# Performance work log

Measured on AMD Instinct MI355X. Metric: run time of the kernel, lower is better.

Reference implementation:

```python
import jax, jax.numpy as jnp
import numpy as np

TEMPERATURE = 0.5
EPS = 1e-12  # matches torch F.normalize clamp_min


def setup_inputs() -> dict:
    key = jax.random.key(0)
    k1, k2 = jax.random.split(key)
    N, D, C = 8192, 128, 64
    out_1 = jax.random.normal(k1, (N, D), dtype=jnp.float32)
    label = jax.random.randint(k2, (N,), 0, C, dtype=jnp.int64)
    return {"out_1": out_1, "label": label}


def reference(out_1, label):
    N = out_1.shape[0]
    # L2 normalize rows (F.normalize with eps clamp)
    norm = jnp.maximum(jnp.linalg.norm(out_1, axis=-1, keepdims=True), EPS)
    x = out_1 / norm
    # exp-scaled cosine similarity matrix [N, N]
    sim = jnp.exp(jnp.matmul(x, x.T) / TEMPERATURE)
    not_diag = 1.0 - jnp.eye(N, dtype=sim.dtype)
    # negatives: all off-diagonal entries per row
    negative_sim = jnp.sum(sim * not_diag, axis=-1)
    # positives: same label, excluding self; mean per row
    pos_mask = (label[:, None] == label[None, :]).astype(sim.dtype) * not_diag
    pos_count = jnp.sum(pos_mask, axis=-1)
    pos_sim = jnp.sum(sim * pos_mask, axis=-1) / pos_count
    return jnp.mean(-jnp.log(pos_sim / negative_sim))
```

## Files before the change

### kernel.cpp

```cpp
#include <hip/hip_runtime.h>
#include <hip/hip_bf16.h>
#include <stdint.h>

typedef __attribute__((ext_vector_type(8))) __bf16 bf16x8;
typedef __attribute__((ext_vector_type(16))) float floatx16;

#if __has_builtin(__builtin_amdgcn_exp2f)
#define EXP2F(x) __builtin_amdgcn_exp2f(x)
#else
#define EXP2F(x) exp2f(x)
#endif

#define GAS __attribute__((address_space(1)))
#define LAS __attribute__((address_space(3)))

#define SCALE_SQRT 1.69864359f
#define JCH 8

__global__ __launch_bounds__(256) void k_prep(const float* __restrict__ x,
                                              const int* __restrict__ raw,
                                              ushort* __restrict__ xb,
                                              int* __restrict__ lab, int N) {
  const int row = (blockIdx.x * 256 + threadIdx.x) >> 6;
  const int lane = threadIdx.x & 63;
  if (row >= N) return;
  const int probe = raw[2 * lane + 1];
  const bool is64 = (__ballot(probe != 0) == 0ull);
  const float2 v = ((const float2*)(x + (size_t)row * 128))[lane];
  float ss = v.x * v.x + v.y * v.y;
#pragma unroll
  for (int m = 1; m < 64; m <<= 1) ss += __shfl_xor(ss, m, 64);
  const float rn = SCALE_SQRT / fmaxf(sqrtf(ss), 1e-12f);
  __hip_bfloat162 o;
  o.x = __float2bfloat16(v.x * rn);
  o.y = __float2bfloat16(v.y * rn);
  ((__hip_bfloat162*)xb)[row * 64 + lane] = o;
  if (lane == 0) lab[row] = is64 ? raw[2 * row] : raw[row];
}

__global__ __launch_bounds__(256, 2) void k_sim(const ushort* __restrict__ xb,
                                                const int* __restrict__ lab,
                                                float* __restrict__ pneg,
                                                float* __restrict__ ppos,
                                                int N, int jpb) {
  __shared__ ushort ldsB[2][64 * 128];
  const int tid = threadIdx.x;
  const int lane = tid & 63;
  const int wv = tid >> 6;
  const int l31 = lane & 31, g2 = lane >> 5;
  const int l15 = lane & 15, g4 = lane >> 4;
  const int i0 = blockIdx.y * 128;
  const int c = blockIdx.x;
  const int jt0 = c * jpb;

  {
    const int j0 = jt0 * 64;
#pragma unroll
    for (int it = 0; it < 4; ++it) {
      const int r0 = it * 16 + wv * 4;
      const int lr = r0 + g4;
      const int kb = l15 ^ (lr & 15);
      const ushort* gp = xb + (size_t)(j0 + lr) * 128 + kb * 8;
      __builtin_amdgcn_global_load_lds((GAS void*)gp, (LAS void*)&ldsB[0][r0 * 128], 16, 0, 0);
    }
  }

  const int arow = i0 + wv * 32 + l31;
  bf16x8 af[8];
#pragma unroll
  for (int kt = 0; kt < 8; ++kt)
    af[kt] = *(const bf16x8*)(xb + (size_t)arow * 128 + (kt * 2 + g2) * 8);

  int li[16];
  float neg[16], pos[16];
#pragma unroll
  for (int r = 0; r < 16; ++r) {
    li[r] = lab[i0 + wv * 32 + (r & 3) + 8 * (r >> 2) + 4 * g2];
    neg[r] = 0.0f;
    pos[r] = 0.0f;
  }
  __syncthreads();

  for (int t = 0; t < jpb; ++t) {
    const int j0 = (jt0 + t) * 64;
    const int buf = t & 1;
    if (t + 1 < jpb) {
      const int jn = j0 + 64;
#pragma unroll
      for (int it = 0; it < 4; ++it) {
        const int r0 = it * 16 + wv * 4;
        const int lr = r0 + g4;
        const int kb = l15 ^ (lr & 15);
        const ushort* gp = xb + (size_t)(jn + lr) * 128 + kb * 8;
        __builtin_amdgcn_global_load_lds((GAS void*)gp, (LAS void*)&ldsB[buf ^ 1][r0 * 128], 16, 0, 0);
      }
    }
    const int lj0 = lab[j0 + l31];
    const int lj1 = lab[j0 + 32 + l31];

    floatx16 acc[2];
    acc[0] = (floatx16)(0.0f);
    acc[1] = (floatx16)(0.0f);
    __builtin_amdgcn_s_setprio(1);
#pragma unroll
    for (int kt = 0; kt < 8; ++kt) {
#pragma unroll
      for (int h = 0; h < 2; ++h) {
        const int brow = h * 32 + l31;
        const int bkb = (kt * 2 + g2) ^ (brow & 15);
        const bf16x8 bfr = *(const bf16x8*)&ldsB[buf][brow * 128 + bkb * 8];
        acc[h] = __builtin_amdgcn_mfma_f32_32x32x16_bf16(af[kt], bfr, acc[h], 0, 0, 0);
      }
    }
    __builtin_amdgcn_s_setprio(0);

    const int dlt = j0 - i0;
    const bool diag = ((unsigned)dlt < 128u);
    auto epi = [&](bool DG) {
#pragma unroll
      for (int h = 0; h < 2; ++h) {
        const int lj = h ? lj1 : lj0;
        const int jc = h * 32 + l31 + dlt;
#pragma unroll
        for (int r = 0; r < 16; ++r) {
          float e = EXP2F(acc[h][r]);
          if (DG) {
            const int ir = wv * 32 + (r & 3) + 8 * (r >> 2) + 4 * g2;
            if (ir == jc) e = 0.0f;
          }
          neg[r] += e;
          pos[r] += (li[r] == lj) ? e : 0.0f;
        }
      }
    };
    if (diag) epi(true); else epi(false);
    __syncthreads();
  }

#pragma unroll
  for (int r = 0; r < 16; ++r) {
    float n = neg[r], p = pos[r];
#pragma unroll
    for (int m = 1; m < 32; m <<= 1) {
      n += __shfl_xor(n, m, 64);
      p += __shfl_xor(p, m, 64);
    }
    if (l31 == 0) {
      const int row = i0 + wv * 32 + (r & 3) + 8 * (r >> 2) + 4 * g2;
      pneg[(size_t)c * N + row] = n;
      ppos[(size_t)c * N + row] = p;
    }
  }
}

__global__ __launch_bounds__(256) void k_final(const float* __restrict__ pneg,
                                               const float* __restrict__ ppos,
                                               const int* __restrict__ lab,
                                               double* __restrict__ partial, int N) {
  __shared__ int h[64];
  __shared__ double wsum[4];
  const int tid = threadIdx.x;
  if (tid < 64) h[tid] = 0;
  __syncthreads();
  for (int i = tid; i < N; i += 256) atomicAdd(&h[lab[i] & 63], 1);
  __syncthreads();
  const int r = blockIdx.x * 256 + tid;
  double v = 0.0;
  if (r < N) {
    float n = 0.0f, p = 0.0f;
#pragma unroll
    for (int cc = 0; cc < JCH; ++cc) {
      n += pneg[(size_t)cc * N + r];
      p += ppos[(size_t)cc * N + r];
    }
    const float cnt = (float)(h[lab[r] & 63] - 1);
    v = (double)logf(n * cnt / p);
  }
#pragma unroll
  for (int m = 1; m < 64; m <<= 1) v += __shfl_xor(v, m, 64);
  if ((tid & 63) == 0) wsum[tid >> 6] = v;
  __syncthreads();
  if (tid == 0) partial[blockIdx.x] = wsum[0] + wsum[1] + wsum[2] + wsum[3];
}

__global__ __launch_bounds__(64) void k_write(const double* __restrict__ partial,
                                              float* __restrict__ out, int nfb, int N) {
  const int l = threadIdx.x;
  double v = 0.0;
  for (int i = l; i < nfb; i += 64) v += partial[i];
#pragma unroll
  for (int m = 1; m < 64; m <<= 1) v += __shfl_xor(v, m, 64);
  if (l == 0) out[0] = (float)(v / (double)N);
}

extern "C" void kernel_launch(void* const* d_in, const int* in_sizes, int n_in,
                              void* d_out, int out_size, void* d_ws, size_t ws_size,
                              hipStream_t stream) {
  const float* x = (const float*)d_in[0];
  const int* raw_label = (const int*)d_in[1];
  const int N = in_sizes[1];
  char* ws = (char*)d_ws;
  ushort* xb = (ushort*)ws;
  float* pneg = (float*)(ws + (size_t)N * 128 * 2);
  float* ppos = pneg + (size_t)JCH * N;
  int* lab = (int*)(ppos + (size_t)JCH * N);
  double* partial = (double*)(lab + N);
  float* out = (float*)d_out;

  const int jpb = (N / 64) / JCH;
  const int nfb = (N + 255) / 256;

  k_prep<<<dim3(N / 4), dim3(256), 0, stream>>>(x, raw_label, xb, lab, N);
  k_sim<<<dim3(JCH, N / 128), dim3(256), 0, stream>>>(xb, lab, pneg, ppos, N, jpb);
  k_final<<<dim3(nfb), dim3(256), 0, stream>>>(pneg, ppos, lab, partial, N);
  k_write<<<dim3(1), dim3(64), 0, stream>>>(partial, out, nfb, N);
}
```

Before: 98.06 us.

## Exploit symmetry of similarity matrix by computing only upper-triangular tile pairs

```diff
diff --git a/kernel.cpp b/kernel.cpp
--- a/kernel.cpp
+++ b/kernel.cpp
@@ -15,7 +15,6 @@
 #define LAS __attribute__((address_space(3)))
 
 #define SCALE_SQRT 1.69864359f
-#define JCH 8
 
 __global__ __launch_bounds__(256) void k_prep(const float* __restrict__ x,
                                               const int* __restrict__ raw,
@@ -42,27 +41,29 @@
                                                 const int* __restrict__ lab,
                                                 float* __restrict__ pneg,
                                                 float* __restrict__ ppos,
-                                                int N, int jpb) {
-  __shared__ ushort ldsB[2][64 * 128];
+                                                int N) {
+  __shared__ ushort ldsB[128 * 128];
   const int tid = threadIdx.x;
   const int lane = tid & 63;
   const int wv = tid >> 6;
   const int l31 = lane & 31, g2 = lane >> 5;
   const int l15 = lane & 15, g4 = lane >> 4;
-  const int i0 = blockIdx.y * 128;
-  const int c = blockIdx.x;
-  const int jt0 = c * jpb;
-
-  {
-    const int j0 = jt0 * 64;
-#pragma unroll
-    for (int it = 0; it < 4; ++it) {
-      const int r0 = it * 16 + wv * 4;
-      const int lr = r0 + g4;
-      const int kb = l15 ^ (lr & 15);
-      const ushort* gp = xb + (size_t)(j0 + lr) * 128 + kb * 8;
-      __builtin_amdgcn_global_load_lds((GAS void*)gp, (LAS void*)&ldsB[0][r0 * 128], 16, 0, 0);
-    }
+
+  const int bid = blockIdx.x;
+  int u = (int)((sqrtf(8.0f * (float)bid + 1.0f) - 1.0f) * 0.5f);
+  while ((u + 1) * (u + 2) / 2 <= bid) ++u;
+  while (u * (u + 1) / 2 > bid) --u;
+  const int s = bid - u * (u + 1) / 2;
+  const int i0 = s * 128;
+  const int jb0 = u * 128;
+
+#pragma unroll
+  for (int it = 0; it < 8; ++it) {
+    const int r0 = it * 16 + wv * 4;
+    const int lr = r0 + g4;
+    const int kb = l15 ^ (lr & 15);
+    const ushort* gp = xb + (size_t)(jb0 + lr) * 128 + kb * 8;
+    __builtin_amdgcn_global_load_lds((GAS void*)gp, (LAS void*)&ldsB[r0 * 128], 16, 0, 0);
   }
 
   const int arow = i0 + wv * 32 + l31;
@@ -79,22 +80,13 @@
     neg[r] = 0.0f;
     pos[r] = 0.0f;
   }
-  __syncthreads();
-
-  for (int t = 0; t < jpb; ++t) {
-    const int j0 = (jt0 + t) * 64;
-    const int buf = t & 1;
-    if (t + 1 < jpb) {
-      const int jn = j0 + 64;
-#pragma unroll
-      for (int it = 0; it < 4; ++it) {
-        const int r0 = it * 16 + wv * 4;
-        const int lr = r0 + g4;
-        const int kb = l15 ^ (lr & 15);
-        const ushort* gp = xb + (size_t)(jn + lr) * 128 + kb * 8;
-        __builtin_amdgcn_global_load_lds((GAS void*)gp, (LAS void*)&ldsB[buf ^ 1][r0 * 128], 16, 0, 0);
-      }
-    }
+  const bool offd = (u != s);
+  __syncthreads();
+
+  float cnT[2][2], cpT[2][2];
+#pragma unroll
+  for (int tile = 0; tile < 2; ++tile) {
+    const int j0 = jb0 + tile * 64;
     const int lj0 = lab[j0 + l31];
     const int lj1 = lab[j0 + 32 + l31];
 
@@ -106,17 +98,31 @@
     for (int kt = 0; kt < 8; ++kt) {
 #pragma unroll
       for (int h = 0; h < 2; ++h) {
-        const int brow = h * 32 + l31;
+        const int brow = tile * 64 + h * 32 + l31;
         const int bkb = (kt * 2 + g2) ^ (brow & 15);
-        const bf16x8 bfr = *(const bf16x8*)&ldsB[buf][brow * 128 + bkb * 8];
+        const bf16x8 bfr = *(const bf16x8*)&ldsB[brow * 128 + bkb * 8];
         acc[h] = __builtin_amdgcn_mfma_f32_32x32x16_bf16(af[kt], bfr, acc[h], 0, 0, 0);
       }
     }
     __builtin_amdgcn_s_setprio(0);
 
-    const int dlt = j0 - i0;
-    const bool diag = ((unsigned)dlt < 128u);
-    auto epi = [&](bool DG) {
+    float cn0 = 0.0f, cn1 = 0.0f, cp0 = 0.0f, cp1 = 0.0f;
+    if (offd) {
+#pragma unroll
+      for (int h = 0; h < 2; ++h) {
+        const int lj = h ? lj1 : lj0;
+#pragma unroll
+        for (int r = 0; r < 16; ++r) {
+          const float e = EXP2F(acc[h][r]);
+          const bool mt = (li[r] == lj);
+          neg[r] += e;
+          pos[r] += mt ? e : 0.0f;
+          if (h) { cn1 += e; cp1 += mt ? e : 0.0f; }
+          else   { cn0 += e; cp0 += mt ? e : 0.0f; }
+        }
+      }
+    } else {
+      const int dlt = tile * 64;
 #pragma unroll
       for (int h = 0; h < 2; ++h) {
         const int lj = h ? lj1 : lj0;
@@ -124,17 +130,15 @@
 #pragma unroll
         for (int r = 0; r < 16; ++r) {
           float e = EXP2F(acc[h][r]);
-          if (DG) {
-            const int ir = wv * 32 + (r & 3) + 8 * (r >> 2) + 4 * g2;
-            if (ir == jc) e = 0.0f;
-          }
+          const int ir = wv * 32 + (r & 3) + 8 * (r >> 2) + 4 * g2;
+          if (ir == jc) e = 0.0f;
           neg[r] += e;
           pos[r] += (li[r] == lj) ? e : 0.0f;
         }
       }
-    };
-    if (diag) epi(true); else epi(false);
-    __syncthreads();
+    }
+    cnT[tile][0] = cn0; cnT[tile][1] = cn1;
+    cpT[tile][0] = cp0; cpT[tile][1] = cp1;
   }
 
 #pragma unroll
@@ -147,16 +151,46 @@
     }
     if (l31 == 0) {
       const int row = i0 + wv * 32 + (r & 3) + 8 * (r >> 2) + 4 * g2;
-      pneg[(size_t)c * N + row] = n;
-      ppos[(size_t)c * N + row] = p;
-    }
+      pneg[(size_t)u * N + row] = n;
+      ppos[(size_t)u * N + row] = p;
+    }
+  }
+
+  if (offd) {
+    __syncthreads();
+    float* cb = (float*)ldsB;
+#pragma unroll
+    for (int tile = 0; tile < 2; ++tile) {
+#pragma unroll
+      for (int h = 0; h < 2; ++h) {
+        float a = cnT[tile][h] + __shfl_xor(cnT[tile][h], 32, 64);
+        float b = cpT[tile][h] + __shfl_xor(cpT[tile][h], 32, 64);
+        if (lane < 32) {
+          cb[(((wv * 2 + tile) * 2 + h) * 2 + 0) * 32 + l31] = a;
+          cb[(((wv * 2 + tile) * 2 + h) * 2 + 1) * 32 + l31] = b;
+        }
+      }
+    }
+    __syncthreads();
+    const int c5 = tid & 31;
+    const int np = (tid >> 5) & 1;
+    const int h = (tid >> 6) & 1;
+    const int t = (tid >> 7) & 1;
+    float v = 0.0f;
+#pragma unroll
+    for (int w = 0; w < 4; ++w)
+      v += cb[(((w * 2 + t) * 2 + h) * 2 + np) * 32 + c5];
+    const int jrow = jb0 + t * 64 + h * 32 + c5;
+    if (np == 0) pneg[(size_t)s * N + jrow] = v;
+    else         ppos[(size_t)s * N + jrow] = v;
   }
 }
 
 __global__ __launch_bounds__(256) void k_final(const float* __restrict__ pneg,
                                                const float* __restrict__ ppos,
                                                const int* __restrict__ lab,
-                                               double* __restrict__ partial, int N) {
+                                               double* __restrict__ partial,
+                                               int N, int nstrip) {
   __shared__ int h[64];
   __shared__ double wsum[4];
   const int tid = threadIdx.x;
@@ -168,8 +202,8 @@
   double v = 0.0;
   if (r < N) {
     float n = 0.0f, p = 0.0f;
-#pragma unroll
-    for (int cc = 0; cc < JCH; ++cc) {
+#pragma unroll 8
+    for (int cc = 0; cc < nstrip; ++cc) {
       n += pneg[(size_t)cc * N + r];
       p += ppos[(size_t)cc * N + r];
     }
@@ -199,19 +233,20 @@
   const float* x = (const float*)d_in[0];
   const int* raw_label = (const int*)d_in[1];
   const int N = in_sizes[1];
+  const int nstrip = N / 128;
   char* ws = (char*)d_ws;
   ushort* xb = (ushort*)ws;
   float* pneg = (float*)(ws + (size_t)N * 128 * 2);
-  float* ppos = pneg + (size_t)JCH * N;
-  int* lab = (int*)(ppos + (size_t)JCH * N);
+  float* ppos = pneg + (size_t)nstrip * N;
+  int* lab = (int*)(ppos + (size_t)nstrip * N);
   double* partial = (double*)(lab + N);
   float* out = (float*)d_out;
 
-  const int jpb = (N / 64) / JCH;
+  const int pairs = nstrip * (nstrip + 1) / 2;
   const int nfb = (N + 255) / 256;
 
   k_prep<<<dim3(N / 4), dim3(256), 0, stream>>>(x, raw_label, xb, lab, N);
-  k_sim<<<dim3(JCH, N / 128), dim3(256), 0, stream>>>(xb, lab, pneg, ppos, N, jpb);
-  k_final<<<dim3(nfb), dim3(256), 0, stream>>>(pneg, ppos, lab, partial, N);
+  k_sim<<<dim3(pairs), dim3(256), 0, stream>>>(xb, lab, pneg, ppos, N);
+  k_final<<<dim3(nfb), dim3(256), 0, stream>>>(pneg, ppos, lab, partial, N, nstrip);
   k_write<<<dim3(1), dim3(64), 0, stream>>>(partial, out, nfb, N);
 }
```

Measured after the change: 101.5 us. +3.5%, slower.

## Pack labels to bytes, vectorize accumulators, raise occupancy and j-split count

Applied to the files above, without the earlier changes.

```diff
diff --git a/kernel.cpp b/kernel.cpp
--- a/kernel.cpp
+++ b/kernel.cpp
@@ -15,12 +15,13 @@
 #define LAS __attribute__((address_space(3)))
 
 #define SCALE_SQRT 1.69864359f
-#define JCH 8
+#define JCH 32
 
 __global__ __launch_bounds__(256) void k_prep(const float* __restrict__ x,
                                               const int* __restrict__ raw,
                                               ushort* __restrict__ xb,
-                                              int* __restrict__ lab, int N) {
+                                              unsigned char* __restrict__ lab8,
+                                              int N) {
   const int row = (blockIdx.x * 256 + threadIdx.x) >> 6;
   const int lane = threadIdx.x & 63;
   if (row >= N) return;
@@ -35,13 +36,12 @@
   o.x = __float2bfloat16(v.x * rn);
   o.y = __float2bfloat16(v.y * rn);
   ((__hip_bfloat162*)xb)[row * 64 + lane] = o;
-  if (lane == 0) lab[row] = is64 ? raw[2 * row] : raw[row];
-}
-
-__global__ __launch_bounds__(256, 2) void k_sim(const ushort* __restrict__ xb,
-                                                const int* __restrict__ lab,
-                                                float* __restrict__ pneg,
-                                                float* __restrict__ ppos,
+  if (lane == 0) lab8[row] = (unsigned char)(is64 ? raw[2 * row] : raw[row]);
+}
+
+__global__ __launch_bounds__(256, 4) void k_sim(const ushort* __restrict__ xb,
+                                                const unsigned char* __restrict__ lab8,
+                                                float2* __restrict__ ppart,
                                                 int N, int jpb) {
   __shared__ ushort ldsB[2][64 * 128];
   const int tid = threadIdx.x;
@@ -71,14 +71,13 @@
   for (int kt = 0; kt < 8; ++kt)
     af[kt] = *(const bf16x8*)(xb + (size_t)arow * 128 + (kt * 2 + g2) * 8);
 
-  int li[16];
-  float neg[16], pos[16];
-#pragma unroll
-  for (int r = 0; r < 16; ++r) {
-    li[r] = lab[i0 + wv * 32 + (r & 3) + 8 * (r >> 2) + 4 * g2];
-    neg[r] = 0.0f;
-    pos[r] = 0.0f;
-  }
+  const uint* lab32 = (const uint*)lab8;
+  uint liw[4];
+#pragma unroll
+  for (int q = 0; q < 4; ++q)
+    liw[q] = lab32[(i0 + wv * 32 + 8 * q + 4 * g2) >> 2];
+
+  floatx16 vneg = (floatx16)(0.0f), vpos = (floatx16)(0.0f);
   __syncthreads();
 
   for (int t = 0; t < jpb; ++t) {
@@ -95,42 +94,39 @@
         __builtin_amdgcn_global_load_lds((GAS void*)gp, (LAS void*)&ldsB[buf ^ 1][r0 * 128], 16, 0, 0);
       }
     }
-    const int lj0 = lab[j0 + l31];
-    const int lj1 = lab[j0 + 32 + l31];
-
-    floatx16 acc[2];
-    acc[0] = (floatx16)(0.0f);
-    acc[1] = (floatx16)(0.0f);
+    const int lj0 = lab8[j0 + l31];
+    const int lj1 = lab8[j0 + 32 + l31];
+
+    floatx16 acc0 = (floatx16)(0.0f), acc1 = (floatx16)(0.0f);
     __builtin_amdgcn_s_setprio(1);
 #pragma unroll
     for (int kt = 0; kt < 8; ++kt) {
-#pragma unroll
-      for (int h = 0; h < 2; ++h) {
-        const int brow = h * 32 + l31;
-        const int bkb = (kt * 2 + g2) ^ (brow & 15);
-        const bf16x8 bfr = *(const bf16x8*)&ldsB[buf][brow * 128 + bkb * 8];
-        acc[h] = __builtin_amdgcn_mfma_f32_32x32x16_bf16(af[kt], bfr, acc[h], 0, 0, 0);
-      }
+      const int br0 = l31;
+      const int br1 = 32 + l31;
+      const bf16x8 b0 = *(const bf16x8*)&ldsB[buf][br0 * 128 + (((kt * 2 + g2) ^ (br0 & 15)) * 8)];
+      const bf16x8 b1 = *(const bf16x8*)&ldsB[buf][br1 * 128 + (((kt * 2 + g2) ^ (br1 & 15)) * 8)];
+      acc0 = __builtin_amdgcn_mfma_f32_32x32x16_bf16(af[kt], b0, acc0, 0, 0, 0);
+      acc1 = __builtin_amdgcn_mfma_f32_32x32x16_bf16(af[kt], b1, acc1, 0, 0, 0);
     }
     __builtin_amdgcn_s_setprio(0);
 
     const int dlt = j0 - i0;
     const bool diag = ((unsigned)dlt < 128u);
+    const int jc0 = l31 + dlt;
+    const int jc1 = 32 + l31 + dlt;
     auto epi = [&](bool DG) {
 #pragma unroll
-      for (int h = 0; h < 2; ++h) {
-        const int lj = h ? lj1 : lj0;
-        const int jc = h * 32 + l31 + dlt;
-#pragma unroll
-        for (int r = 0; r < 16; ++r) {
-          float e = EXP2F(acc[h][r]);
-          if (DG) {
-            const int ir = wv * 32 + (r & 3) + 8 * (r >> 2) + 4 * g2;
-            if (ir == jc) e = 0.0f;
-          }
-          neg[r] += e;
-          pos[r] += (li[r] == lj) ? e : 0.0f;
+      for (int r = 0; r < 16; ++r) {
+        const int lr = (liw[r >> 2] >> ((r & 3) * 8)) & 255;
+        float e0 = EXP2F(acc0[r]);
+        float e1 = EXP2F(acc1[r]);
+        if (DG) {
+          const int ir = wv * 32 + (r & 3) + 8 * (r >> 2) + 4 * g2;
+          if (ir == jc0) e0 = 0.0f;
+          if (ir == jc1) e1 = 0.0f;
         }
+        vneg[r] += e0 + e1;
+        vpos[r] += ((lr == lj0) ? e0 : 0.0f) + ((lr == lj1) ? e1 : 0.0f);
       }
     };
     if (diag) epi(true); else epi(false);
@@ -139,7 +135,7 @@
 
 #pragma unroll
   for (int r = 0; r < 16; ++r) {
-    float n = neg[r], p = pos[r];
+    float n = vneg[r], p = vpos[r];
 #pragma unroll
     for (int m = 1; m < 32; m <<= 1) {
       n += __shfl_xor(n, m, 64);
@@ -147,33 +143,33 @@
     }
     if (l31 == 0) {
       const int row = i0 + wv * 32 + (r & 3) + 8 * (r >> 2) + 4 * g2;
-      pneg[(size_t)c * N + row] = n;
-      ppos[(size_t)c * N + row] = p;
-    }
-  }
-}
-
-__global__ __launch_bounds__(256) void k_final(const float* __restrict__ pneg,
-                                               const float* __restrict__ ppos,
-                                               const int* __restrict__ lab,
-                                               double* __restrict__ partial, int N) {
+      ppart[(size_t)c * N + row] = float2{n, p};
+    }
+  }
+}
+
+__global__ __launch_bounds__(256) void k_final(const float2* __restrict__ ppart,
+                                               const unsigned char* __restrict__ lab8,
+                                               double* __restrict__ partial,
+                                               int N, int nplanes) {
   __shared__ int h[64];
   __shared__ double wsum[4];
   const int tid = threadIdx.x;
   if (tid < 64) h[tid] = 0;
   __syncthreads();
-  for (int i = tid; i < N; i += 256) atomicAdd(&h[lab[i] & 63], 1);
+  for (int i = tid; i < N; i += 256) atomicAdd(&h[lab8[i] & 63], 1);
   __syncthreads();
   const int r = blockIdx.x * 256 + tid;
   double v = 0.0;
   if (r < N) {
     float n = 0.0f, p = 0.0f;
-#pragma unroll
-    for (int cc = 0; cc < JCH; ++cc) {
-      n += pneg[(size_t)cc * N + r];
-      p += ppos[(size_t)cc * N + r];
-    }
-    const float cnt = (float)(h[lab[r] & 63] - 1);
+#pragma unroll 8
+    for (int cc = 0; cc < nplanes; ++cc) {
+      const float2 w = ppart[(size_t)cc * N + r];
+      n += w.x;
+      p += w.y;
+    }
+    const float cnt = (float)(h[lab8[r] & 63] - 1);
     v = (double)logf(n * cnt / p);
   }
 #pragma unroll
@@ -201,17 +197,16 @@
   const int N = in_sizes[1];
   char* ws = (char*)d_ws;
   ushort* xb = (ushort*)ws;
-  float* pneg = (float*)(ws + (size_t)N * 128 * 2);
-  float* ppos = pneg + (size_t)JCH * N;
-  int* lab = (int*)(ppos + (size_t)JCH * N);
-  double* partial = (double*)(lab + N);
+  float2* ppart = (float2*)(ws + (size_t)N * 128 * 2);
+  unsigned char* lab8 = (unsigned char*)(ppart + (size_t)JCH * N);
+  double* partial = (double*)(lab8 + ((N + 7) & ~7));
   float* out = (float*)d_out;
 
   const int jpb = (N / 64) / JCH;
   const int nfb = (N + 255) / 256;
 
-  k_prep<<<dim3(N / 4), dim3(256), 0, stream>>>(x, raw_label, xb, lab, N);
-  k_sim<<<dim3(JCH, N / 128), dim3(256), 0, stream>>>(xb, lab, pneg, ppos, N, jpb);
-  k_final<<<dim3(nfb), dim3(256), 0, stream>>>(pneg, ppos, lab, partial, N);
+  k_prep<<<dim3(N / 4), dim3(256), 0, stream>>>(x, raw_label, xb, lab8, N);
+  k_sim<<<dim3(JCH, N / 128), dim3(256), 0, stream>>>(xb, lab8, ppart, N, jpb);
+  k_final<<<dim3(nfb), dim3(256), 0, stream>>>(ppart, lab8, partial, N, JCH);
   k_write<<<dim3(1), dim3(64), 0, stream>>>(partial, out, nfb, N);
 }
```

After: 182.8 us. +86.4%, slower.
